# Kernel optimization log

Hardware: AMD Instinct MI355X
Metric: run time of the kernel (lower is better)

Reference implementation:

```python
import jax, jax.numpy as jnp
import numpy as np

N_TOKENS = 32768
DIM = 2048
N_EXPERTS = 256
N_GROUPS = 8
N_LIMITED_GROUPS = 4
TOP_K = 8
ROUTE_SCALE = 2.5


def setup_inputs() -> dict:
    key = jax.random.key(0)
    k1, k2, k3, k4 = jax.random.split(key, 4)
    x = jax.random.normal(k1, (N_TOKENS, DIM), dtype=jnp.float32)
    w1 = jax.random.normal(k2, (N_EXPERTS, DIM), dtype=jnp.float32) * (DIM ** -0.5)
    b_lin = jax.random.normal(k3, (N_EXPERTS,), dtype=jnp.float32) * 0.02
    bias = jax.random.normal(k4, (N_EXPERTS,), dtype=jnp.float32) * 0.02
    return {"x": x, "w1": w1, "b_lin": b_lin, "bias": bias}


def reference(x, w1, b_lin, bias):
    n = x.shape[0]
    # gate GEMM: [N, dim] x [dim, E] -> [N, E]
    logits = jnp.einsum("nd,ed->ne", x, w1) + b_lin
    # sigmoid scoring with L1 normalization
    s = jax.nn.sigmoid(logits)
    s = s / jnp.sum(s, axis=-1, keepdims=True)
    # routing-correction bias (torch code adds it in place, so it is also in the
    # gathered values via the original_scores alias)
    s = s + bias
    original_scores = s
    # group-limited masking: keep only top n_limited_groups groups (amax score,
    # since use_bias=True)
    g = s.reshape(n, N_GROUPS, N_EXPERTS // N_GROUPS)
    group_scores = jnp.max(g, axis=-1)                      # [N, G]
    _, gidx = jax.lax.top_k(group_scores, N_LIMITED_GROUPS)  # [N, Glim]
    keep = jnp.zeros((n, N_GROUPS), dtype=bool).at[
        jnp.arange(n)[:, None], gidx].set(True)
    masked = jnp.where(keep[:, :, None], g, -jnp.inf).reshape(n, N_EXPERTS)
    # final top-k over masked scores, gather from (bias-added) original scores
    _, indices = jax.lax.top_k(masked, TOP_K)               # [N, k]
    values = jnp.take_along_axis(original_scores, indices, axis=1) * ROUTE_SCALE
    return values.astype(x.dtype), indices
```

## Files before the change

### kernel.cpp

```cpp
#include <hip/hip_runtime.h>
#include <math.h>

#define NTOK   32768
#define DIM    2048
#define NE     256
#define NG     8
#define GSZ    32
#define NLIM   4
#define TOPK   8
#define RSCALE 2.5f
#define TAU    4e-7f

#define BT      32
#define THREADS 256
#define KT      16
#define NKT     (DIM / KT)
#define WOFF    262144
#define TILE_B  16384

typedef __bf16 bf16x8 __attribute__((ext_vector_type(8)));
typedef float  f32x16 __attribute__((ext_vector_type(16)));

typedef const __attribute__((address_space(1))) void GASV;
typedef __attribute__((address_space(3))) void LASV;

__device__ __forceinline__ void gload16(const void* g, void* l) {
    __builtin_amdgcn_global_load_lds((GASV*)g, (LASV*)l, 16, 0, 0);
}

__global__ __launch_bounds__(256) void wsplit_kernel(
    const float* __restrict__ w1, unsigned int* __restrict__ wt)
{
    const int g  = blockIdx.x * 256 + threadIdx.x;
    const int e  = g & 255;
    const int hi = (g >> 8) & 1;
    const int p  = (g >> 9) & 1;
    const int kt = g >> 10;
    const float* src = w1 + (size_t)e * DIM + kt * 16 + hi * 8;

    uint4 o;
    unsigned int w[4];
#pragma unroll
    for (int q = 0; q < 4; ++q) {
        const float v0 = src[2 * q], v1 = src[2 * q + 1];
        const unsigned int u0 = __float_as_uint(v0);
        const unsigned int u1 = __float_as_uint(v1);
        if (p == 0) {
            w[q] = (u0 >> 16) | (u1 & 0xFFFF0000u);
        } else {
            const float r0 = v0 - __uint_as_float(u0 & 0xFFFF0000u);
            const float r1 = v1 - __uint_as_float(u1 & 0xFFFF0000u);
            w[q] = (__float_as_uint(r0) >> 16) |
                   (__float_as_uint(r1) & 0xFFFF0000u);
        }
    }
    o.x = w[0]; o.y = w[1]; o.z = w[2]; o.w = w[3];
    *(uint4*)(wt + (size_t)g * 4) = o;
}

__global__ __launch_bounds__(THREADS, 4) void router_pass1(
    const float* __restrict__ x, const unsigned int* __restrict__ wt,
    const float* __restrict__ b_lin, const float* __restrict__ bias,
    float* __restrict__ out_vals, float* __restrict__ out_idx,
    int* __restrict__ wsI)
{
    __shared__ union {
        struct {
            alignas(16) char B[2][TILE_B];
            unsigned short xs[2][2][32][16];
        } t;
        float sc[32 * 260];
    } sm;

    const int tid  = threadIdx.x;
    const int lane = tid & 63;
    const int wn   = tid >> 6;
    const int l31  = lane & 31;
    const int hi   = lane >> 5;
    const int t0   = blockIdx.x * BT;

    const int xtok = tid >> 3, xk2 = tid & 7;
    const float2* xg = (const float2*)(x + (size_t)(t0 + xtok) * DIM) + xk2;

    const char* wsrc = (const char*)wt;

    auto STAGE = [&](char* ldsbase, int kt) {
#pragma unroll
        for (int q = 0; q < 4; ++q) {
            const int chunk = wn * 4 + q;
            gload16(wsrc + (size_t)kt * TILE_B + chunk * 1024 + lane * 16,
                    ldsbase + chunk * 1024);
        }
    };
    auto XWRITE = [&](int b, float2 v) {
        const unsigned int u0 = __float_as_uint(v.x);
        const unsigned int u1 = __float_as_uint(v.y);
        const unsigned int hp = (u0 >> 16) | (u1 & 0xFFFF0000u);
        const float r0 = v.x - __uint_as_float(u0 & 0xFFFF0000u);
        const float r1 = v.y - __uint_as_float(u1 & 0xFFFF0000u);
        const unsigned int rp = (__float_as_uint(r0) >> 16) |
                                (__float_as_uint(r1) & 0xFFFF0000u);
        *(unsigned int*)&sm.t.xs[b][0][xtok][xk2 * 2] = hp;
        *(unsigned int*)&sm.t.xs[b][1][xtok][xk2 * 2] = rp;
    };

    f32x16 acc[2] = {};

    float2 xv = xg[0];
    __builtin_amdgcn_sched_barrier(0);
    STAGE(sm.t.B[0], 0);
    __builtin_amdgcn_sched_barrier(0);
    asm volatile("s_waitcnt vmcnt(4)");
    __builtin_amdgcn_sched_barrier(0);
    XWRITE(0, xv);
    __syncthreads();

    for (int kt = 0; kt < NKT; ++kt) {
        const int cur = kt & 1, nxt = cur ^ 1;
        if (kt + 1 < NKT) {
            xv = xg[(kt + 1) * 8];
            __builtin_amdgcn_sched_barrier(0);
            STAGE(sm.t.B[nxt], kt + 1);
            __builtin_amdgcn_sched_barrier(0);
        }

        bf16x8 ah = *(const bf16x8*)&sm.t.xs[cur][0][l31][hi * 8];
        bf16x8 ar = *(const bf16x8*)&sm.t.xs[cur][1][l31][hi * 8];
#pragma unroll
        for (int ni = 0; ni < 2; ++ni) {
            const int e = wn * 64 + ni * 32 + l31;
            const char* pb = sm.t.B[cur] + ((0 * 2 + hi) * 256 + e) * 16;
            const char* pr = sm.t.B[cur] + ((1 * 2 + hi) * 256 + e) * 16;
            bf16x8 bh = *(const bf16x8*)pb;
            bf16x8 br = *(const bf16x8*)pr;
            acc[ni] = __builtin_amdgcn_mfma_f32_32x32x16_bf16(ah, bh, acc[ni], 0, 0, 0);
            acc[ni] = __builtin_amdgcn_mfma_f32_32x32x16_bf16(ah, br, acc[ni], 0, 0, 0);
            acc[ni] = __builtin_amdgcn_mfma_f32_32x32x16_bf16(ar, bh, acc[ni], 0, 0, 0);
        }

        if (kt + 1 < NKT) {
            asm volatile("s_waitcnt vmcnt(4)");
            __builtin_amdgcn_sched_barrier(0);
            XWRITE(nxt, xv);
        }
        __syncthreads();
    }

    const int tx = tid & 31;
    const int ty = tid >> 5;
    float blv[8], bsv[8];
#pragma unroll
    for (int j = 0; j < 8; ++j) {
        blv[j] = b_lin[tx + 32 * j];
        bsv[j] = bias[tx + 32 * j];
    }

#pragma unroll
    for (int ni = 0; ni < 2; ++ni) {
#pragma unroll
        for (int r = 0; r < 16; ++r) {
            const int row = (r & 3) + 8 * (r >> 2) + 4 * hi;
            const int e   = wn * 64 + ni * 32 + l31;
            sm.sc[row * 260 + e] = acc[ni][r];
        }
    }
    __syncthreads();

#pragma unroll
    for (int i = 0; i < 4; ++i) {
        const int row = ty * 4 + i;
        float s8[8];
        float psum = 0.0f;
#pragma unroll
        for (int j = 0; j < 8; ++j) {
            const float lg = sm.sc[row * 260 + tx + 32 * j] + blv[j];
            const float s = 1.0f / (1.0f + expf(-lg));
            s8[j] = s;
            psum += s;
        }
#pragma unroll
        for (int m = 1; m <= 16; m <<= 1) psum += __shfl_xor(psum, m);
#pragma unroll
        for (int j = 0; j < 8; ++j) s8[j] = s8[j] / psum + bsv[j];

        float gm[8];
#pragma unroll
        for (int j = 0; j < 8; ++j) gm[j] = s8[j];
#pragma unroll
        for (int m = 1; m <= 16; m <<= 1)
#pragma unroll
            for (int j = 0; j < 8; ++j)
                gm[j] = fmaxf(gm[j], __shfl_xor(gm[j], m));

        unsigned keep = 0u;
        float g4v = 0.0f, g5v = 0.0f;
#pragma unroll
        for (int r = 0; r < 5; ++r) {
            float bv = -1e30f; int bg = 0;
#pragma unroll
            for (int g = 0; g < 8; ++g)
                if (!((keep >> g) & 1) && gm[g] > bv) { bv = gm[g]; bg = g; }
            if (r < 4) { keep |= 1u << bg; g4v = bv; }
            else g5v = bv;
        }
        float margin = g4v - g5v;

#pragma unroll
        for (int j = 0; j < 8; ++j)
            if (!((keep >> j) & 1)) s8[j] = -1e30f;

        float tv[9]; int te[9];
#pragma unroll
        for (int r = 0; r < 9; ++r) {
            float bv = -1e30f; int bj = 8;
#pragma unroll
            for (int j = 0; j < 8; ++j)
                if (s8[j] > bv) { bv = s8[j]; bj = j; }
            int be = (bj < 8) ? (tx + 32 * bj) : 9999;
#pragma unroll
            for (int m = 1; m <= 16; m <<= 1) {
                const float ov = __shfl_xor(bv, m);
                const int   oe = __shfl_xor(be, m);
                if (ov > bv || (ov == bv && oe < be)) { bv = ov; be = oe; }
            }
            tv[r] = bv; te[r] = be;
            if (r < 8 && (be & 31) == tx) s8[be >> 5] = -1e30f;
        }
#pragma unroll
        for (int r = 0; r < 8; ++r) margin = fminf(margin, tv[r] - tv[r + 1]);

        if (tx == 0) {
            const int t = t0 + row;
            const int base = t * TOPK;
#pragma unroll
            for (int r = 0; r < 8; ++r) {
                out_vals[base + r] = tv[r] * RSCALE;
                out_idx[base + r]  = (float)te[r];
            }
            if (margin < TAU) {
                const int slot = atomicAdd(&wsI[0], 1);
                if (slot < 60000) wsI[4 + slot] = t;
            }
        }
    }
}

__global__ __launch_bounds__(256, 1) void router_pass2(
    const float* __restrict__ x, const float* __restrict__ w1,
    const float* __restrict__ b_lin, const float* __restrict__ bias,
    float* __restrict__ out_vals, float* __restrict__ out_idx,
    const int* __restrict__ wsI)
{
    __shared__ double xrow[DIM];
    __shared__ double red[256];
    __shared__ double sc[NE];

    const int tid = threadIdx.x;
    const int count = min(wsI[0], 60000);
    const int* list = wsI + 4;
    const float4* x4 = (const float4*)x;
    const float4* w4 = (const float4*)w1;

    for (int li = blockIdx.x; li < count; li += gridDim.x) {
        const int t = list[li];
        __syncthreads();
#pragma unroll
        for (int q = 0; q < 2; ++q) {
            const int id = tid + 256 * q;
            const float4 v = x4[t * 512 + id];
            xrow[id * 4 + 0] = (double)v.x;
            xrow[id * 4 + 1] = (double)v.y;
            xrow[id * 4 + 2] = (double)v.z;
            xrow[id * 4 + 3] = (double)v.w;
        }
        __syncthreads();

        const int e = tid;
        double a0 = 0.0, a1 = 0.0, a2 = 0.0, a3 = 0.0;
#pragma unroll 2
        for (int k4 = 0; k4 < 512; k4 += 4) {
#pragma unroll
            for (int z = 0; z < 4; ++z) {
                const float4 wv = w4[e * 512 + k4 + z];
                double* ac = (z == 0) ? &a0 : (z == 1) ? &a1 : (z == 2) ? &a2 : &a3;
                *ac = fma(xrow[(k4 + z) * 4 + 0], (double)wv.x, *ac);
                *ac = fma(xrow[(k4 + z) * 4 + 1], (double)wv.y, *ac);
                *ac = fma(xrow[(k4 + z) * 4 + 2], (double)wv.z, *ac);
                *ac = fma(xrow[(k4 + z) * 4 + 3], (double)wv.w, *ac);
            }
        }
        const double lg = ((a0 + a1) + (a2 + a3)) + (double)b_lin[e];
        const double s = 1.0 / (1.0 + exp(-lg));
        red[tid] = s;
        __syncthreads();
        for (int off = 128; off > 0; off >>= 1) {
            if (tid < off) red[tid] += red[tid + off];
            __syncthreads();
        }
        sc[e] = s / red[0] + (double)bias[e];
        __syncthreads();

        if (tid == 0) {
            double gmax[NG];
            for (int g = 0; g < NG; ++g) {
                double mx = -INFINITY;
                for (int q = 0; q < GSZ; ++q) {
                    const double v = sc[g * GSZ + q];
                    mx = (v > mx) ? v : mx;
                }
                gmax[g] = mx;
            }
            unsigned keep = 0u;
            for (int r = 0; r < NLIM; ++r) {
                int best = 0; double bv = -INFINITY;
                for (int g = 0; g < NG; ++g) {
                    if (keep & (1u << g)) continue;
                    if (gmax[g] > bv) { bv = gmax[g]; best = g; }
                }
                keep |= 1u << best;
            }
            double tv[TOPK]; int ti[TOPK];
            for (int r = 0; r < TOPK; ++r) { tv[r] = -INFINITY; ti[r] = NE; }
            for (int g = 0; g < NG; ++g) {
                if (!(keep & (1u << g))) continue;
                for (int q = 0; q < GSZ; ++q) {
                    const int ee = g * GSZ + q;
                    const double v = sc[ee];
                    if (v > tv[TOPK - 1]) {
                        int p = TOPK - 1;
                        while (p > 0 && v > tv[p - 1]) {
                            tv[p] = tv[p - 1]; ti[p] = ti[p - 1]; --p;
                        }
                        tv[p] = v; ti[p] = ee;
                    }
                }
            }
            const int base = t * TOPK;
            for (int r = 0; r < TOPK; ++r) {
                out_vals[base + r] = (float)(tv[r] * (double)RSCALE);
                out_idx[base + r]  = (float)ti[r];
            }
        }
    }
}

extern "C" void kernel_launch(void* const* d_in, const int* in_sizes, int n_in,
                              void* d_out, int out_size, void* d_ws, size_t ws_size,
                              hipStream_t stream) {
    const float* x     = (const float*)d_in[0];
    const float* w1    = (const float*)d_in[1];
    const float* b_lin = (const float*)d_in[2];
    const float* bias  = (const float*)d_in[3];
    float* out_vals = (float*)d_out;
    float* out_idx  = (float*)d_out + (size_t)NTOK * TOPK;

    int* wsI = (int*)d_ws;
    unsigned int* wt = (unsigned int*)((char*)d_ws + WOFF);

    hipMemsetAsync(d_ws, 0, 16, stream);
    wsplit_kernel<<<dim3(512), 256, 0, stream>>>(w1, wt);
    router_pass1<<<dim3(NTOK / BT), THREADS, 0, stream>>>(
        x, wt, b_lin, bias, out_vals, out_idx, wsI);
    router_pass2<<<dim3(256), 256, 0, stream>>>(
        x, w1, b_lin, bias, out_vals, out_idx, (const int*)d_ws);
}
```

Measured before the change: 269.7 us.

## Load weight fragments directly into registers instead of staging through LDS

Weight tiles are now read straight from global memory into per-wave registers, two register sets deep, rather than copied into a double-buffered LDS tile with global_load_lds. The loop is unrolled by two with ping-pong register buffers, and the full __syncthreads is replaced by an LDS-only wait plus s_barrier. This removes the LDS traffic and footprint for B, which should allow higher occupancy. In exchange, each wave issues its own global loads, the weight reads across blocks depend on L2 hits, and register pressure grows.

Result: no change. 269.7 us (+0.0%).

```diff
diff --git a/kernel.cpp b/kernel.cpp
--- a/kernel.cpp
+++ b/kernel.cpp
@@ -20,13 +20,6 @@
 
 typedef __bf16 bf16x8 __attribute__((ext_vector_type(8)));
 typedef float  f32x16 __attribute__((ext_vector_type(16)));
-
-typedef const __attribute__((address_space(1))) void GASV;
-typedef __attribute__((address_space(3))) void LASV;
-
-__device__ __forceinline__ void gload16(const void* g, void* l) {
-    __builtin_amdgcn_global_load_lds((GASV*)g, (LASV*)l, 16, 0, 0);
-}
 
 __global__ __launch_bounds__(256) void wsplit_kernel(
     const float* __restrict__ w1, unsigned int* __restrict__ wt)
@@ -65,10 +58,7 @@
     int* __restrict__ wsI)
 {
     __shared__ union {
-        struct {
-            alignas(16) char B[2][TILE_B];
-            unsigned short xs[2][2][32][16];
-        } t;
+        unsigned short xs[2][2][32][16];
         float sc[32 * 260];
     } sm;
 
@@ -82,15 +72,15 @@
     const int xtok = tid >> 3, xk2 = tid & 7;
     const float2* xg = (const float2*)(x + (size_t)(t0 + xtok) * DIM) + xk2;
 
-    const char* wsrc = (const char*)wt;
-
-    auto STAGE = [&](char* ldsbase, int kt) {
-#pragma unroll
-        for (int q = 0; q < 4; ++q) {
-            const int chunk = wn * 4 + q;
-            gload16(wsrc + (size_t)kt * TILE_B + chunk * 1024 + lane * 16,
-                    ldsbase + chunk * 1024);
-        }
+    const char* wb = (const char*)wt + hi * 4096 + (wn * 64 + l31) * 16;
+
+    auto LOADB = [&](bf16x8 B[2][2], int kt) {
+#pragma unroll
+        for (int ni = 0; ni < 2; ++ni)
+#pragma unroll
+            for (int p = 0; p < 2; ++p)
+                B[ni][p] = *(const bf16x8*)(wb + (size_t)kt * TILE_B +
+                                            ni * 512 + p * 8192);
     };
     auto XWRITE = [&](int b, float2 v) {
         const unsigned int u0 = __float_as_uint(v.x);
@@ -100,51 +90,54 @@
         const float r1 = v.y - __uint_as_float(u1 & 0xFFFF0000u);
         const unsigned int rp = (__float_as_uint(r0) >> 16) |
                                 (__float_as_uint(r1) & 0xFFFF0000u);
-        *(unsigned int*)&sm.t.xs[b][0][xtok][xk2 * 2] = hp;
-        *(unsigned int*)&sm.t.xs[b][1][xtok][xk2 * 2] = rp;
+        *(unsigned int*)&sm.xs[b][0][xtok][xk2 * 2] = hp;
+        *(unsigned int*)&sm.xs[b][1][xtok][xk2 * 2] = rp;
     };
 
     f32x16 acc[2] = {};
 
+    auto COMP = [&](bf16x8 B[2][2], int cur) {
+        bf16x8 ah = *(const bf16x8*)&sm.xs[cur][0][l31][hi * 8];
+        bf16x8 ar = *(const bf16x8*)&sm.xs[cur][1][l31][hi * 8];
+#pragma unroll
+        for (int ni = 0; ni < 2; ++ni) {
+            acc[ni] = __builtin_amdgcn_mfma_f32_32x32x16_bf16(ah, B[ni][0], acc[ni], 0, 0, 0);
+            acc[ni] = __builtin_amdgcn_mfma_f32_32x32x16_bf16(ah, B[ni][1], acc[ni], 0, 0, 0);
+            acc[ni] = __builtin_amdgcn_mfma_f32_32x32x16_bf16(ar, B[ni][0], acc[ni], 0, 0, 0);
+        }
+    };
+    auto BARRIER = [&]() {
+        __builtin_amdgcn_sched_barrier(0);
+        asm volatile("s_waitcnt lgkmcnt(0)");
+        __builtin_amdgcn_sched_barrier(0);
+        __builtin_amdgcn_s_barrier();
+        __builtin_amdgcn_sched_barrier(0);
+    };
+
+    bf16x8 BA[2][2], BB[2][2];
+    float2 xo, xe;
+
+    LOADB(BA, 0);
     float2 xv = xg[0];
-    __builtin_amdgcn_sched_barrier(0);
-    STAGE(sm.t.B[0], 0);
-    __builtin_amdgcn_sched_barrier(0);
-    asm volatile("s_waitcnt vmcnt(4)");
-    __builtin_amdgcn_sched_barrier(0);
     XWRITE(0, xv);
+    LOADB(BB, 1);
+    xo = xg[8];
+    BARRIER();
+
+    for (int kt = 0; kt < NKT; kt += 2) {
+        if (kt + 1 < NKT) XWRITE(1, xo);
+        if (kt + 2 < NKT) xe = xg[(kt + 2) * 8];
+        COMP(BA, 0);
+        if (kt + 2 < NKT) LOADB(BA, kt + 2);
+        BARRIER();
+        if (kt + 2 < NKT) XWRITE(0, xe);
+        if (kt + 3 < NKT) xo = xg[(kt + 3) * 8];
+        COMP(BB, 1);
+        if (kt + 3 < NKT) LOADB(BB, kt + 3);
+        BARRIER();
+    }
+
     __syncthreads();
-
-    for (int kt = 0; kt < NKT; ++kt) {
-        const int cur = kt & 1, nxt = cur ^ 1;
-        if (kt + 1 < NKT) {
-            xv = xg[(kt + 1) * 8];
-            __builtin_amdgcn_sched_barrier(0);
-            STAGE(sm.t.B[nxt], kt + 1);
-            __builtin_amdgcn_sched_barrier(0);
-        }
-
-        bf16x8 ah = *(const bf16x8*)&sm.t.xs[cur][0][l31][hi * 8];
-        bf16x8 ar = *(const bf16x8*)&sm.t.xs[cur][1][l31][hi * 8];
-#pragma unroll
-        for (int ni = 0; ni < 2; ++ni) {
-            const int e = wn * 64 + ni * 32 + l31;
-            const char* pb = sm.t.B[cur] + ((0 * 2 + hi) * 256 + e) * 16;
-            const char* pr = sm.t.B[cur] + ((1 * 2 + hi) * 256 + e) * 16;
-            bf16x8 bh = *(const bf16x8*)pb;
-            bf16x8 br = *(const bf16x8*)pr;
-            acc[ni] = __builtin_amdgcn_mfma_f32_32x32x16_bf16(ah, bh, acc[ni], 0, 0, 0);
-            acc[ni] = __builtin_amdgcn_mfma_f32_32x32x16_bf16(ah, br, acc[ni], 0, 0, 0);
-            acc[ni] = __builtin_amdgcn_mfma_f32_32x32x16_bf16(ar, bh, acc[ni], 0, 0, 0);
-        }
-
-        if (kt + 1 < NKT) {
-            asm volatile("s_waitcnt vmcnt(4)");
-            __builtin_amdgcn_sched_barrier(0);
-            XWRITE(nxt, xv);
-        }
-        __syncthreads();
-    }
 
     const int tx = tid & 31;
     const int ty = tid >> 5;
```
